# Kernel tuning notes

Hardware: AMD Instinct MI355X
Metric: run time of the kernel (lower is better)

The kernel has to match this reference:

```python
import jax, jax.numpy as jnp
import numpy as np

NEG_INF = -1e38

def wkv(w, u, k, v):
    """Numerically-stable RWKV-4 WKV recurrence.
    w, u: [C] (log-space decay / first-token bonus)
    k, v: [B, T, C]
    returns y: [B, T, C]
    """
    B, T, C = k.shape

    def step(carry, kv):
        p, q, o = carry          # numerator state, denominator state, running log-max; each [B, C]
        kt, vt = kv              # [B, C]
        # output at t (includes the u-boosted current token)
        no = jnp.maximum(o, u + kt)
        A = jnp.exp(o - no)
        Bt = jnp.exp(u + kt - no)
        y = (A * p + Bt * vt) / (A * q + Bt)
        # state update (decay by w, absorb current token)
        no2 = jnp.maximum(w + o, kt)
        A2 = jnp.exp(w + o - no2)
        B2 = jnp.exp(kt - no2)
        return (A2 * p + B2 * vt, A2 * q + B2, no2), y

    init = (jnp.zeros((B, C), k.dtype), jnp.zeros((B, C), k.dtype),
            jnp.full((B, C), NEG_INF, k.dtype))
    kT = jnp.swapaxes(k, 0, 1)   # [T, B, C]
    vT = jnp.swapaxes(v, 0, 1)
    _, ys = jax.lax.scan(step, init, (kT, vT))
    return jnp.swapaxes(ys, 0, 1)


def setup_inputs() -> dict:
    key = jax.random.key(0)
    ks = jax.random.split(key, 10)
    B, T, C = 8, 4096, 512
    scale = 1.0 / np.sqrt(C)
    return {
        "x": jax.random.normal(ks[0], (B, T, C), jnp.float32),
        "spatial_decay": jax.random.normal(ks[1], (C,), jnp.float32),
        "spatial_first": jax.random.normal(ks[2], (C,), jnp.float32),
        "mix_k": jax.random.uniform(ks[3], (1, 1, C), jnp.float32),
        "mix_v": jax.random.uniform(ks[4], (1, 1, C), jnp.float32),
        "mix_r": jax.random.uniform(ks[5], (1, 1, C), jnp.float32),
        "wk": jax.random.normal(ks[6], (C, C), jnp.float32) * scale,
        "wv": jax.random.normal(ks[7], (C, C), jnp.float32) * scale,
        "wr": jax.random.normal(ks[8], (C, C), jnp.float32) * scale,
        "wo": jax.random.normal(ks[9], (C, C), jnp.float32) * scale,
    }


def reference(x, spatial_decay, spatial_first, mix_k, mix_v, mix_r, wk, wv, wr, wo):
    B, T, C = x.shape
    # time_shift: xx[t] = x[t-1], xx[0] = 0  (ZeroPad2d((0,0,1,-1)))
    xx = jnp.pad(x, ((0, 0), (1, 0), (0, 0)))[:, :-1]
    xk = x * mix_k + xx * (1.0 - mix_k)
    xv = x * mix_v + xx * (1.0 - mix_v)
    xr = x * mix_r + xx * (1.0 - mix_r)
    k = jnp.einsum('btc,cd->btd', xk, wk)
    v = jnp.einsum('btc,cd->btd', xv, wv)
    r = jnp.einsum('btc,cd->btd', xr, wr)
    sr = jax.nn.sigmoid(r)
    y = wkv(spatial_decay / T, spatial_first / T, k, v)
    return jnp.einsum('btc,cd->btd', sr * y, wo)
```

## Files before the change

kernel.cpp:

```cpp
#include <hip/hip_runtime.h>

#define BB 8
#define TT 4096
#define CC 512
#define MM (BB * TT)
#define SS 128
#define LL 32

typedef short short8 __attribute__((ext_vector_type(8)));
typedef unsigned short ushort8 __attribute__((ext_vector_type(8)));
typedef float f32x4 __attribute__((ext_vector_type(4)));

__device__ __forceinline__ unsigned short f2bf(float f) {
    unsigned int u = __float_as_uint(f);
    u += 0x7FFFu + ((u >> 16) & 1u);
    return (unsigned short)(u >> 16);
}
__device__ __forceinline__ float bf2f(unsigned short h) {
    return __uint_as_float(((unsigned int)h) << 16);
}

__device__ __forceinline__ void gl_lds16(const void* g, void* l) {
    __builtin_amdgcn_global_load_lds(
        (__attribute__((address_space(1))) void*)(unsigned long long)g,
        (__attribute__((address_space(3))) void*)(unsigned int)(unsigned long long)l,
        16, 0, 0);
}

__device__ __forceinline__ ushort8 pack8(f32x4 a, f32x4 b) {
    ushort8 r;
    r[0] = f2bf(a.x); r[1] = f2bf(a.y); r[2] = f2bf(a.z); r[3] = f2bf(a.w);
    r[4] = f2bf(b.x); r[5] = f2bf(b.y); r[6] = f2bf(b.z); r[7] = f2bf(b.w);
    return r;
}

__global__ __launch_bounds__(256) void transpose_w(
    const float* __restrict__ wk, const float* __restrict__ wv,
    const float* __restrict__ wr, const float* __restrict__ wo,
    unsigned short* __restrict__ wT) {
    __shared__ float t[64][65];
    const int which = blockIdx.z;
    const float* src = (which == 0) ? wk : (which == 1) ? wv : (which == 2) ? wr : wo;
    const int k0 = blockIdx.y * 64;
    const int n0 = blockIdx.x * 64;
    const int r = threadIdx.x >> 6;
    const int c = threadIdx.x & 63;
#pragma unroll
    for (int p = 0; p < 16; ++p)
        t[p * 4 + r][c] = src[(size_t)(k0 + p * 4 + r) * CC + n0 + c];
    __syncthreads();
    unsigned short* dst = wT + (size_t)which * (CC * CC);
#pragma unroll
    for (int p = 0; p < 16; ++p)
        dst[(size_t)(n0 + p * 4 + r) * CC + k0 + c] = f2bf(t[c][p * 4 + r]);
}

__global__ __launch_bounds__(256) void mix_kvr(
    const float* __restrict__ x,
    const float* __restrict__ mixk, const float* __restrict__ mixv,
    const float* __restrict__ mixr,
    unsigned short* __restrict__ kx, unsigned short* __restrict__ vx,
    unsigned short* __restrict__ rx) {
    const int idx = blockIdx.x * 256 + threadIdx.x;
    const int row = idx >> 6;
    const int ch  = (idx & 63) * 8;
    const int t   = row & (TT - 1);
    const size_t off = (size_t)row * CC + ch;
    const float* xr = x + off;

    const f32x4 zero4 = {0.f, 0.f, 0.f, 0.f};
    const f32x4 one4  = {1.f, 1.f, 1.f, 1.f};

    f32x4 xc0 = ((const f32x4*)xr)[0];
    f32x4 xc1 = ((const f32x4*)xr)[1];
    f32x4 xp0 = zero4, xp1 = zero4;
    if (t != 0) {
        xp0 = ((const f32x4*)(xr - CC))[0];
        xp1 = ((const f32x4*)(xr - CC))[1];
    }

    f32x4 m0, m1;
    m0 = ((const f32x4*)(mixk + ch))[0];
    m1 = ((const f32x4*)(mixk + ch))[1];
    *(ushort8*)(kx + off) = pack8(xc0 * m0 + xp0 * (one4 - m0),
                                  xc1 * m1 + xp1 * (one4 - m1));
    m0 = ((const f32x4*)(mixv + ch))[0];
    m1 = ((const f32x4*)(mixv + ch))[1];
    *(ushort8*)(vx + off) = pack8(xc0 * m0 + xp0 * (one4 - m0),
                                  xc1 * m1 + xp1 * (one4 - m1));
    m0 = ((const f32x4*)(mixr + ch))[0];
    m1 = ((const f32x4*)(mixr + ch))[1];
    *(ushort8*)(rx + off) = pack8(xc0 * m0 + xp0 * (one4 - m0),
                                  xc1 * m1 + xp1 * (one4 - m1));
}

template <bool F32OUT>
__device__ __forceinline__ void gemm_body(
    const unsigned short* __restrict__ A,
    const unsigned short* __restrict__ Bw,
    void* __restrict__ OutP, const int sig,
    const int pm, const int pn) {
    __shared__ unsigned short As[3][128 * 32];
    __shared__ unsigned short Bs[3][256 * 32];

    const int tid = threadIdx.x;
    const int ar = tid >> 2;
    const int cg = (tid & 3) ^ ((tid >> 3) & 3);
    const unsigned short* agA = A  + (size_t)(pm * 128 + ar) * CC + cg * 8;
    const unsigned short* agB = Bw + (size_t)(pn * 256 + ar) * CC + cg * 8;

    const int w = tid >> 6, lane = tid & 63;
    const int wr = w >> 1, wc = w & 1;
    const int q = lane >> 4, l16 = lane & 15;
    const int sw = (q ^ ((l16 >> 1) & 3)) * 8;

    f32x4 acc[4][8];
#pragma unroll
    for (int i = 0; i < 4; i++)
#pragma unroll
        for (int j = 0; j < 8; j++) acc[i][j] = (f32x4){0.f, 0.f, 0.f, 0.f};

#define STG(bi, k0) do {                                                        \
    gl_lds16(agA + (k0), &As[bi][tid * 8]);                                     \
    gl_lds16(agA + (size_t)64 * CC + (k0), &As[bi][(256 + tid) * 8]);           \
    gl_lds16(agB + (k0),                    &Bs[bi][(0 * 256 + tid) * 8]);      \
    gl_lds16(agB + (size_t)64  * CC + (k0), &Bs[bi][(1 * 256 + tid) * 8]);      \
    gl_lds16(agB + (size_t)128 * CC + (k0), &Bs[bi][(2 * 256 + tid) * 8]);      \
    gl_lds16(agB + (size_t)192 * CC + (k0), &Bs[bi][(3 * 256 + tid) * 8]);      \
} while (0)

    STG(0, 0);
    STG(1, 32);

#pragma unroll
    for (int kt = 0; kt < 16; ++kt) {
        const int bi = kt % 3;
        if (kt + 2 < 16) STG((kt + 2) % 3, (kt + 2) * 32);

        if (kt < 14)       asm volatile("s_waitcnt vmcnt(12)" ::: "memory");
        else if (kt == 14) asm volatile("s_waitcnt vmcnt(6)" ::: "memory");
        else               asm volatile("s_waitcnt vmcnt(0)" ::: "memory");
        __builtin_amdgcn_s_barrier();

        short8 a[4], b[8];
#pragma unroll
        for (int i = 0; i < 4; i++)
            a[i] = *(const short8*)&As[bi][(wr * 64 + i * 16 + l16) * 32 + sw];
#pragma unroll
        for (int j = 0; j < 8; j++)
            b[j] = *(const short8*)&Bs[bi][(wc * 128 + j * 16 + l16) * 32 + sw];
        asm volatile("s_waitcnt lgkmcnt(0)" ::: "memory");
        __builtin_amdgcn_s_barrier();

        __builtin_amdgcn_s_setprio(1);
#pragma unroll
        for (int i = 0; i < 4; i++)
#pragma unroll
            for (int j = 0; j < 8; j++)
                acc[i][j] = __builtin_amdgcn_mfma_f32_16x16x32_bf16(a[i], b[j], acc[i][j], 0, 0, 0);
        __builtin_amdgcn_s_setprio(0);
    }
#undef STG

    const size_t rb = (size_t)pm * 128 + wr * 64;
    const int nb = pn * 256 + wc * 128;
    if constexpr (F32OUT) {
        float* Out = (float*)OutP;
#pragma unroll
        for (int i = 0; i < 4; i++)
#pragma unroll
            for (int j = 0; j < 8; j++)
#pragma unroll
                for (int ii = 0; ii < 4; ii++) {
                    const int m = i * 16 + q * 4 + ii;
                    const int n = nb + j * 16 + l16;
                    Out[(rb + m) * CC + n] = acc[i][j][ii];
                }
    } else {
        unsigned short* Out = (unsigned short*)OutP;
#pragma unroll
        for (int i = 0; i < 4; i++)
#pragma unroll
            for (int j = 0; j < 8; j++)
#pragma unroll
                for (int ii = 0; ii < 4; ii++) {
                    const int m = i * 16 + q * 4 + ii;
                    const int n = nb + j * 16 + l16;
                    float val = acc[i][j][ii];
                    if (sig) val = 1.0f / (1.0f + __expf(-val));
                    Out[(rb + m) * CC + n] = f2bf(val);
                }
    }
}

__global__ __launch_bounds__(256, 2) void gemm_kvr3(
    const unsigned short* __restrict__ wT,
    const unsigned short* __restrict__ A0, const unsigned short* __restrict__ A1,
    const unsigned short* __restrict__ A2,
    unsigned short* __restrict__ O0, unsigned short* __restrict__ O1,
    unsigned short* __restrict__ O2) {
    const int z = blockIdx.y;
    const int lin = blockIdx.x;
    const int wg = (lin & 7) * 64 + (lin >> 3);
    const int pm = wg >> 1, pn = wg & 1;
    const unsigned short* A = (z == 0) ? A0 : (z == 1) ? A1 : A2;
    unsigned short* O = (z == 0) ? O0 : (z == 1) ? O1 : O2;
    gemm_body<false>(A, wT + (size_t)z * (CC * CC), O, z == 2, pm, pn);
}

__global__ __launch_bounds__(256, 2) void gemm_out(
    const unsigned short* __restrict__ zb, const unsigned short* __restrict__ woT,
    float* __restrict__ out) {
    const int lin = blockIdx.x;
    const int wg = (lin & 7) * 64 + (lin >> 3);
    gemm_body<true>(zb, woT, out, 0, wg >> 1, wg & 1);
}

__global__ __launch_bounds__(256) void wkv_part1(
    const unsigned short* __restrict__ kb, const unsigned short* __restrict__ vb,
    const float* __restrict__ sd,
    float* __restrict__ sp_, float* __restrict__ sq_, float* __restrict__ so_) {
    const int idx = blockIdx.x * 256 + threadIdx.x;
    const int c = idx & (CC - 1);
    const int b = (idx >> 9) & (BB - 1);
    const int s = idx >> 12;
    const float w = sd[c] * (1.0f / (float)TT);
    const size_t base = ((size_t)b * TT + (size_t)s * LL) * CC + c;
    const unsigned short* kp = kb + base;
    const unsigned short* vp = vb + base;

    float p = 0.f, q = 0.f, o = -1e38f;
#pragma unroll 8
    for (int i = 0; i < LL; ++i) {
        const float kt = bf2f(kp[(size_t)i * CC]);
        const float vt = bf2f(vp[(size_t)i * CC]);
        const float no2 = fmaxf(w + o, kt);
        const float A2  = __expf(w + o - no2);
        const float B2  = __expf(kt - no2);
        p = A2 * p + B2 * vt;
        q = A2 * q + B2;
        o = no2;
    }
    sp_[idx] = p; sq_[idx] = q; so_[idx] = o;
}

__global__ __launch_bounds__(256) void wkv_part2(
    const float* __restrict__ sd,
    float* __restrict__ sp_, float* __restrict__ sq_, float* __restrict__ so_) {
    const int idx = blockIdx.x * 256 + threadIdx.x;
    const int c = idx & (CC - 1);
    const float wL = sd[c] * ((float)LL / (float)TT);

    float p = 0.f, q = 0.f, o = -1e38f;
    float lp = sp_[idx], lq = sq_[idx], lo = so_[idx];
    for (int s = 0; s < SS; ++s) {
        const int off = s * (BB * CC) + idx;
        float nlp = 0.f, nlq = 0.f, nlo = 0.f;
        if (s + 1 < SS) {
            nlp = sp_[off + BB * CC];
            nlq = sq_[off + BB * CC];
            nlo = so_[off + BB * CC];
        }
        sp_[off] = p; sq_[off] = q; so_[off] = o;
        const float no = fmaxf(o + wL, lo);
        const float A  = __expf(o + wL - no);
        const float Bc = __expf(lo - no);
        p = A * p + Bc * lp;
        q = A * q + Bc * lq;
        o = no;
        lp = nlp; lq = nlq; lo = nlo;
    }
}

__global__ __launch_bounds__(256) void wkv_part3(
    const unsigned short* __restrict__ kb, const unsigned short* __restrict__ vb,
    const unsigned short* __restrict__ srb,
    const float* __restrict__ sd, const float* __restrict__ sf,
    const float* __restrict__ sp_, const float* __restrict__ sq_,
    const float* __restrict__ so_,
    unsigned short* __restrict__ zb) {
    const int idx = blockIdx.x * 256 + threadIdx.x;
    const int c = idx & (CC - 1);
    const int b = (idx >> 9) & (BB - 1);
    const int s = idx >> 12;
    const float w = sd[c] * (1.0f / (float)TT);
    const float u = sf[c] * (1.0f / (float)TT);
    const size_t base = ((size_t)b * TT + (size_t)s * LL) * CC + c;
    const unsigned short* kp = kb + base;
    const unsigned short* vp = vb + base;
    const unsigned short* sp = srb + base;
    unsigned short* zp = zb + base;

    float p = sp_[idx], q = sq_[idx], o = so_[idx];
#pragma unroll 4
    for (int i = 0; i < LL; ++i) {
        const float kt = bf2f(kp[(size_t)i * CC]);
        const float vt = bf2f(vp[(size_t)i * CC]);
        const float sr = bf2f(sp[(size_t)i * CC]);

        const float no = fmaxf(o, u + kt);
        const float A  = __expf(o - no);
        const float Bt = __expf(u + kt - no);
        const float y  = (A * p + Bt * vt) / (A * q + Bt);
        zp[(size_t)i * CC] = f2bf(sr * y);

        const float no2 = fmaxf(w + o, kt);
        const float A2  = __expf(w + o - no2);
        const float B2  = __expf(kt - no2);
        p = A2 * p + B2 * vt;
        q = A2 * q + B2;
        o = no2;
    }
}

extern "C" void kernel_launch(void* const* d_in, const int* in_sizes, int n_in,
                              void* d_out, int out_size, void* d_ws, size_t ws_size,
                              hipStream_t stream) {
    const float* x  = (const float*)d_in[0];
    const float* sd = (const float*)d_in[1];
    const float* sf = (const float*)d_in[2];
    const float* mk = (const float*)d_in[3];
    const float* mv = (const float*)d_in[4];
    const float* mr = (const float*)d_in[5];
    const float* wk = (const float*)d_in[6];
    const float* wv = (const float*)d_in[7];
    const float* wr = (const float*)d_in[8];
    const float* wo = (const float*)d_in[9];
    float* out = (float*)d_out;

    char* ws = (char*)d_ws;
    unsigned short* wT = (unsigned short*)ws;
    unsigned short* b1 = wT + (size_t)4 * CC * CC;
    unsigned short* b2 = b1 + (size_t)MM * CC;
    unsigned short* b3 = b2 + (size_t)MM * CC;
    unsigned short* b4 = b3 + (size_t)MM * CC;
    unsigned short* b5 = b4 + (size_t)MM * CC;
    float* sp_ = (float*)(b5 + (size_t)MM * CC);
    float* sq_ = sp_ + (size_t)SS * BB * CC;
    float* so_ = sq_ + (size_t)SS * BB * CC;
    unsigned short* woT = wT + (size_t)3 * CC * CC;
    unsigned short* srS = (unsigned short*)d_out;

    transpose_w<<<dim3(8, 8, 4), 256, 0, stream>>>(wk, wv, wr, wo, wT);

    mix_kvr<<<dim3((MM * CC / 8) / 256), 256, 0, stream>>>(
        x, mk, mv, mr, b1, b2, b3);

    gemm_kvr3<<<dim3(512, 3), 256, 0, stream>>>(wT, b1, b2, b3, b4, b5, srS);

    wkv_part1<<<dim3((SS * BB * CC) / 256), 256, 0, stream>>>(b4, b5, sd, sp_, sq_, so_);
    wkv_part2<<<dim3((BB * CC) / 256), 256, 0, stream>>>(sd, sp_, sq_, so_);
    wkv_part3<<<dim3((SS * BB * CC) / 256), 256, 0, stream>>>(
        b4, b5, srS, sd, sf, sp_, sq_, so_, b1);

    gemm_out<<<dim3(512), 256, 0, stream>>>(b1, woT, out);
}
```

Before: 295.6 us.

## Enlarge GEMM tiles to 256x256 with 8 waves and interleaved LDS staging

Reworks the shared bf16 GEMM body from a 128x256 tile on 4 waves to a 256x256 tile on 8 waves, each wave owning a 128x64 subtile. Global-to-LDS staging of A and B is split and interleaved between two MFMA half-phases. Only one barrier per k-step remains, and the k loop is no longer unrolled. The three kvr GEMMs are flattened into one 1D grid with a new block-swizzle, and the output GEMM uses half as many blocks. This aims for more operand reuse per LDS byte and better overlap of loads with MFMA, at the cost of larger LDS use (about 96 KB per block, likely one block per CU) and fewer blocks to balance the load.

New measurement: 313.6 us. 6.1% more time.

```diff
diff --git a/kernel.cpp b/kernel.cpp
--- a/kernel.cpp
+++ b/kernel.cpp
@@ -100,76 +100,101 @@
     const unsigned short* __restrict__ Bw,
     void* __restrict__ OutP, const int sig,
     const int pm, const int pn) {
-    __shared__ unsigned short As[3][128 * 32];
+    __shared__ unsigned short As[3][256 * 32];
     __shared__ unsigned short Bs[3][256 * 32];
 
     const int tid = threadIdx.x;
-    const int ar = tid >> 2;
     const int cg = (tid & 3) ^ ((tid >> 3) & 3);
-    const unsigned short* agA = A  + (size_t)(pm * 128 + ar) * CC + cg * 8;
-    const unsigned short* agB = Bw + (size_t)(pn * 256 + ar) * CC + cg * 8;
-
-    const int w = tid >> 6, lane = tid & 63;
-    const int wr = w >> 1, wc = w & 1;
+    const unsigned short* agA = A  + (size_t)(pm * 256 + (tid >> 2)) * CC + cg * 8;
+    const unsigned short* agB = Bw + (size_t)(pn * 256 + (tid >> 2)) * CC + cg * 8;
+
+    const int wid = tid >> 6;
+    const int wr = wid >> 2, wc = wid & 3;
+    const int lane = tid & 63;
     const int q = lane >> 4, l16 = lane & 15;
     const int sw = (q ^ ((l16 >> 1) & 3)) * 8;
 
-    f32x4 acc[4][8];
-#pragma unroll
-    for (int i = 0; i < 4; i++)
-#pragma unroll
-        for (int j = 0; j < 8; j++) acc[i][j] = (f32x4){0.f, 0.f, 0.f, 0.f};
-
-#define STG(bi, k0) do {                                                        \
-    gl_lds16(agA + (k0), &As[bi][tid * 8]);                                     \
-    gl_lds16(agA + (size_t)64 * CC + (k0), &As[bi][(256 + tid) * 8]);           \
-    gl_lds16(agB + (k0),                    &Bs[bi][(0 * 256 + tid) * 8]);      \
-    gl_lds16(agB + (size_t)64  * CC + (k0), &Bs[bi][(1 * 256 + tid) * 8]);      \
-    gl_lds16(agB + (size_t)128 * CC + (k0), &Bs[bi][(2 * 256 + tid) * 8]);      \
-    gl_lds16(agB + (size_t)192 * CC + (k0), &Bs[bi][(3 * 256 + tid) * 8]);      \
+    const int aro = (wr * 128 + l16) * 32 + sw;
+    const int bro = (wc * 64 + l16) * 32 + sw;
+
+    f32x4 acc[8][4];
+#pragma unroll
+    for (int i = 0; i < 8; i++)
+#pragma unroll
+        for (int j = 0; j < 4; j++) acc[i][j] = (f32x4){0.f, 0.f, 0.f, 0.f};
+
+#define STG_A(bi_, ke) do {                                                   \
+    gl_lds16(agA + (ke), &As[bi_][tid * 8]);                                  \
+    gl_lds16(agA + (size_t)128 * CC + (ke), &As[bi_][4096 + tid * 8]);        \
 } while (0)
-
-    STG(0, 0);
-    STG(1, 32);
-
-#pragma unroll
-    for (int kt = 0; kt < 16; ++kt) {
-        const int bi = kt % 3;
-        if (kt + 2 < 16) STG((kt + 2) % 3, (kt + 2) * 32);
-
-        if (kt < 14)       asm volatile("s_waitcnt vmcnt(12)" ::: "memory");
-        else if (kt == 14) asm volatile("s_waitcnt vmcnt(6)" ::: "memory");
-        else               asm volatile("s_waitcnt vmcnt(0)" ::: "memory");
+#define STG_B(bi_, ke) do {                                                   \
+    gl_lds16(agB + (ke), &Bs[bi_][tid * 8]);                                  \
+    gl_lds16(agB + (size_t)128 * CC + (ke), &Bs[bi_][4096 + tid * 8]);        \
+} while (0)
+
+    STG_A(0, 0);  STG_B(0, 0);
+    STG_A(1, 32); STG_B(1, 32);
+
+    short8 bfr[4], af[4];
+
+#define KT_PHASES(bi_, DO_STAGE, ke) do {                                     \
+    const int bi2_ = (bi_) + 2 >= 3 ? (bi_) - 1 : (bi_) + 2;                  \
+    if (DO_STAGE) STG_A(bi2_, ke);                                            \
+    _Pragma("unroll")                                                         \
+    for (int j = 0; j < 4; ++j)                                               \
+        bfr[j] = *(const short8*)&Bs[bi_][bro + j * 512];                     \
+    _Pragma("unroll")                                                         \
+    for (int i = 0; i < 4; ++i)                                               \
+        af[i] = *(const short8*)&As[bi_][aro + i * 512];                      \
+    asm volatile("s_waitcnt lgkmcnt(0)" ::: "memory");                        \
+    __builtin_amdgcn_s_setprio(1);                                            \
+    _Pragma("unroll")                                                         \
+    for (int i = 0; i < 4; ++i)                                               \
+        _Pragma("unroll")                                                     \
+        for (int j = 0; j < 4; ++j)                                           \
+            acc[i][j] = __builtin_amdgcn_mfma_f32_16x16x32_bf16(              \
+                af[i], bfr[j], acc[i][j], 0, 0, 0);                           \
+    __builtin_amdgcn_s_setprio(0);                                            \
+    if (DO_STAGE) STG_B(bi2_, ke);                                            \
+    _Pragma("unroll")                                                         \
+    for (int i = 0; i < 4; ++i)                                               \
+        af[i] = *(const short8*)&As[bi_][aro + 2048 + i * 512];               \
+    asm volatile("s_waitcnt lgkmcnt(0)" ::: "memory");                        \
+    __builtin_amdgcn_s_setprio(1);                                            \
+    _Pragma("unroll")                                                         \
+    for (int i = 0; i < 4; ++i)                                               \
+        _Pragma("unroll")                                                     \
+        for (int j = 0; j < 4; ++j)                                           \
+            acc[4 + i][j] = __builtin_amdgcn_mfma_f32_16x16x32_bf16(          \
+                af[i], bfr[j], acc[4 + i][j], 0, 0, 0);                       \
+    __builtin_amdgcn_s_setprio(0);                                            \
+} while (0)
+
+    int bi = 0, ks = 64;
+#pragma unroll 1
+    for (int t = 0; t < 15; ++t) {
+        asm volatile("s_waitcnt vmcnt(4)" ::: "memory");
         __builtin_amdgcn_s_barrier();
-
-        short8 a[4], b[8];
-#pragma unroll
-        for (int i = 0; i < 4; i++)
-            a[i] = *(const short8*)&As[bi][(wr * 64 + i * 16 + l16) * 32 + sw];
-#pragma unroll
-        for (int j = 0; j < 8; j++)
-            b[j] = *(const short8*)&Bs[bi][(wc * 128 + j * 16 + l16) * 32 + sw];
-        asm volatile("s_waitcnt lgkmcnt(0)" ::: "memory");
-        __builtin_amdgcn_s_barrier();
-
-        __builtin_amdgcn_s_setprio(1);
-#pragma unroll
-        for (int i = 0; i < 4; i++)
-#pragma unroll
-            for (int j = 0; j < 8; j++)
-                acc[i][j] = __builtin_amdgcn_mfma_f32_16x16x32_bf16(a[i], b[j], acc[i][j], 0, 0, 0);
-        __builtin_amdgcn_s_setprio(0);
-    }
-#undef STG
-
-    const size_t rb = (size_t)pm * 128 + wr * 64;
-    const int nb = pn * 256 + wc * 128;
+        KT_PHASES(bi, (t < 14), ks);
+        ks += 32;
+        bi = (bi + 1 == 3) ? 0 : bi + 1;
+    }
+    asm volatile("s_waitcnt vmcnt(0)" ::: "memory");
+    __builtin_amdgcn_s_barrier();
+    KT_PHASES(bi, false, 0);
+
+#undef KT_PHASES
+#undef STG_A
+#undef STG_B
+
+    const size_t rb = (size_t)pm * 256 + wr * 128;
+    const int nb = pn * 256 + wc * 64;
     if constexpr (F32OUT) {
         float* Out = (float*)OutP;
 #pragma unroll
-        for (int i = 0; i < 4; i++)
-#pragma unroll
-            for (int j = 0; j < 8; j++)
+        for (int i = 0; i < 8; i++)
+#pragma unroll
+            for (int j = 0; j < 4; j++)
 #pragma unroll
                 for (int ii = 0; ii < 4; ii++) {
                     const int m = i * 16 + q * 4 + ii;
@@ -179,9 +204,9 @@
     } else {
         unsigned short* Out = (unsigned short*)OutP;
 #pragma unroll
-        for (int i = 0; i < 4; i++)
-#pragma unroll
-            for (int j = 0; j < 8; j++)
+        for (int i = 0; i < 8; i++)
+#pragma unroll
+            for (int j = 0; j < 4; j++)
 #pragma unroll
                 for (int ii = 0; ii < 4; ii++) {
                     const int m = i * 16 + q * 4 + ii;
@@ -193,26 +218,27 @@
     }
 }
 
-__global__ __launch_bounds__(256, 2) void gemm_kvr3(
+__global__ __launch_bounds__(512, 2) void gemm_kvr3(
     const unsigned short* __restrict__ wT,
     const unsigned short* __restrict__ A0, const unsigned short* __restrict__ A1,
     const unsigned short* __restrict__ A2,
     unsigned short* __restrict__ O0, unsigned short* __restrict__ O1,
     unsigned short* __restrict__ O2) {
-    const int z = blockIdx.y;
     const int lin = blockIdx.x;
-    const int wg = (lin & 7) * 64 + (lin >> 3);
-    const int pm = wg >> 1, pn = wg & 1;
+    const int wg = (lin & 7) * 96 + (lin >> 3);
+    const int z = wg >> 8;
+    const int r = wg & 255;
+    const int pm = r >> 1, pn = r & 1;
     const unsigned short* A = (z == 0) ? A0 : (z == 1) ? A1 : A2;
     unsigned short* O = (z == 0) ? O0 : (z == 1) ? O1 : O2;
     gemm_body<false>(A, wT + (size_t)z * (CC * CC), O, z == 2, pm, pn);
 }
 
-__global__ __launch_bounds__(256, 2) void gemm_out(
+__global__ __launch_bounds__(512, 2) void gemm_out(
     const unsigned short* __restrict__ zb, const unsigned short* __restrict__ woT,
     float* __restrict__ out) {
     const int lin = blockIdx.x;
-    const int wg = (lin & 7) * 64 + (lin >> 3);
+    const int wg = (lin & 7) * 32 + (lin >> 3);
     gemm_body<true>(zb, woT, out, 0, wg >> 1, wg & 1);
 }
 
@@ -346,12 +372,12 @@
     mix_kvr<<<dim3((MM * CC / 8) / 256), 256, 0, stream>>>(
         x, mk, mv, mr, b1, b2, b3);
 
-    gemm_kvr3<<<dim3(512, 3), 256, 0, stream>>>(wT, b1, b2, b3, b4, b5, srS);
+    gemm_kvr3<<<dim3(768), 512, 0, stream>>>(wT, b1, b2, b3, b4, b5, srS);
 
     wkv_part1<<<dim3((SS * BB * CC) / 256), 256, 0, stream>>>(b4, b5, sd, sp_, sq_, so_);
     wkv_part2<<<dim3((BB * CC) / 256), 256, 0, stream>>>(sd, sp_, sq_, so_);
     wkv_part3<<<dim3((SS * BB * CC) / 256), 256, 0, stream>>>(
         b4, b5, srS, sd, sf, sp_, sq_, so_, b1);
 
-    gemm_out<<<dim3(512), 256, 0, stream>>>(b1, woT, out);
-}
+    gemm_out<<<dim3(256), 512, 0, stream>>>(b1, woT, out);
+}
```

## Parallelize chunk-state scan with Hillis-Steele in LDS; merge weight transpose into mix

Applied to the files above, without the earlier changes.

The serial 128-step cross-chunk state scan, which ran on only 4096 threads, becomes a parallel log-depth inclusive scan in shared memory. Each (batch, channel) pair gets 128 threads, one per chunk, and the associative combine uses doubling decay factors. Separately, the weight transpose and token-mix kernels are merged into one launch to save a kernel launch and let the two overlap. The scan does more total work and adds barriers, and the combine order differs slightly, which may change float rounding.

Result: no change. 299.8 us (+1.4%).

```diff
diff --git a/kernel.cpp b/kernel.cpp
--- a/kernel.cpp
+++ b/kernel.cpp
@@ -34,37 +34,40 @@
     return r;
 }
 
-__global__ __launch_bounds__(256) void transpose_w(
-    const float* __restrict__ wk, const float* __restrict__ wv,
-    const float* __restrict__ wr, const float* __restrict__ wo,
-    unsigned short* __restrict__ wT) {
-    __shared__ float t[64][65];
-    const int which = blockIdx.z;
-    const float* src = (which == 0) ? wk : (which == 1) ? wv : (which == 2) ? wr : wo;
-    const int k0 = blockIdx.y * 64;
-    const int n0 = blockIdx.x * 64;
-    const int r = threadIdx.x >> 6;
-    const int c = threadIdx.x & 63;
-#pragma unroll
-    for (int p = 0; p < 16; ++p)
-        t[p * 4 + r][c] = src[(size_t)(k0 + p * 4 + r) * CC + n0 + c];
-    __syncthreads();
-    unsigned short* dst = wT + (size_t)which * (CC * CC);
-#pragma unroll
-    for (int p = 0; p < 16; ++p)
-        dst[(size_t)(n0 + p * 4 + r) * CC + k0 + c] = f2bf(t[c][p * 4 + r]);
-}
-
-__global__ __launch_bounds__(256) void mix_kvr(
+__global__ __launch_bounds__(256) void prep(
     const float* __restrict__ x,
     const float* __restrict__ mixk, const float* __restrict__ mixv,
     const float* __restrict__ mixr,
+    const float* __restrict__ wk, const float* __restrict__ wv,
+    const float* __restrict__ wr, const float* __restrict__ wo,
+    unsigned short* __restrict__ wT,
     unsigned short* __restrict__ kx, unsigned short* __restrict__ vx,
     unsigned short* __restrict__ rx) {
-    const int idx = blockIdx.x * 256 + threadIdx.x;
+    __shared__ float t[64][65];
+    if (blockIdx.x < 256) {
+        const int bid = blockIdx.x;
+        const int which = bid >> 6;
+        const int rem = bid & 63;
+        const int k0 = (rem >> 3) * 64;
+        const int n0 = (rem & 7) * 64;
+        const float* src = (which == 0) ? wk : (which == 1) ? wv
+                         : (which == 2) ? wr : wo;
+        const int r = threadIdx.x >> 6;
+        const int c = threadIdx.x & 63;
+#pragma unroll
+        for (int p = 0; p < 16; ++p)
+            t[p * 4 + r][c] = src[(size_t)(k0 + p * 4 + r) * CC + n0 + c];
+        __syncthreads();
+        unsigned short* dst = wT + (size_t)which * (CC * CC);
+#pragma unroll
+        for (int p = 0; p < 16; ++p)
+            dst[(size_t)(n0 + p * 4 + r) * CC + k0 + c] = f2bf(t[c][p * 4 + r]);
+        return;
+    }
+    const int idx = (blockIdx.x - 256) * 256 + threadIdx.x;
     const int row = idx >> 6;
     const int ch  = (idx & 63) * 8;
-    const int t   = row & (TT - 1);
+    const int tt  = row & (TT - 1);
     const size_t off = (size_t)row * CC + ch;
     const float* xr = x + off;
 
@@ -74,7 +77,7 @@
     f32x4 xc0 = ((const f32x4*)xr)[0];
     f32x4 xc1 = ((const f32x4*)xr)[1];
     f32x4 xp0 = zero4, xp1 = zero4;
-    if (t != 0) {
+    if (tt != 0) {
         xp0 = ((const f32x4*)(xr - CC))[0];
         xp1 = ((const f32x4*)(xr - CC))[1];
     }
@@ -244,32 +247,49 @@
     sp_[idx] = p; sq_[idx] = q; so_[idx] = o;
 }
 
-__global__ __launch_bounds__(256) void wkv_part2(
+__global__ __launch_bounds__(256) void wkv_scan(
     const float* __restrict__ sd,
     float* __restrict__ sp_, float* __restrict__ sq_, float* __restrict__ so_) {
-    const int idx = blockIdx.x * 256 + threadIdx.x;
-    const int c = idx & (CC - 1);
+    __shared__ float P[2][128], Q[2][128], O[2][128];
+    const int gsub = threadIdx.x >> 7;
+    const int s    = threadIdx.x & 127;
+    const int g    = blockIdx.x * 2 + gsub;
+    const int c    = g & (CC - 1);
     const float wL = sd[c] * ((float)LL / (float)TT);
-
-    float p = 0.f, q = 0.f, o = -1e38f;
-    float lp = sp_[idx], lq = sq_[idx], lo = so_[idx];
-    for (int s = 0; s < SS; ++s) {
-        const int off = s * (BB * CC) + idx;
-        float nlp = 0.f, nlq = 0.f, nlo = 0.f;
-        if (s + 1 < SS) {
-            nlp = sp_[off + BB * CC];
-            nlq = sq_[off + BB * CC];
-            nlo = so_[off + BB * CC];
+    const int stride = BB * CC;
+
+    float p = sp_[s * stride + g];
+    float q = sq_[s * stride + g];
+    float o = so_[s * stride + g];
+    P[gsub][s] = p; Q[gsub][s] = q; O[gsub][s] = o;
+
+    float dec = wL;
+#pragma unroll
+    for (int d = 0; d < 7; ++d) {
+        const int off = 1 << d;
+        __syncthreads();
+        float pl = 0.f, ql = 0.f, ol = -1e38f;
+        if (s >= off) {
+            pl = P[gsub][s - off]; ql = Q[gsub][s - off]; ol = O[gsub][s - off];
         }
-        sp_[off] = p; sq_[off] = q; so_[off] = o;
-        const float no = fmaxf(o + wL, lo);
-        const float A  = __expf(o + wL - no);
-        const float Bc = __expf(lo - no);
-        p = A * p + Bc * lp;
-        q = A * q + Bc * lq;
-        o = no;
-        lp = nlp; lq = nlq; lo = nlo;
-    }
+        __syncthreads();
+        if (s >= off) {
+            const float no = fmaxf(ol + dec, o);
+            const float Al = __expf(ol + dec - no);
+            const float Bc = __expf(o - no);
+            p = Al * pl + Bc * p;
+            q = Al * ql + Bc * q;
+            o = no;
+            P[gsub][s] = p; Q[gsub][s] = q; O[gsub][s] = o;
+        }
+        dec += dec;
+    }
+    __syncthreads();
+    float ep = 0.f, eq = 0.f, eo = -1e38f;
+    if (s > 0) { ep = P[gsub][s - 1]; eq = Q[gsub][s - 1]; eo = O[gsub][s - 1]; }
+    sp_[s * stride + g] = ep;
+    sq_[s * stride + g] = eq;
+    so_[s * stride + g] = eo;
 }
 
 __global__ __launch_bounds__(256) void wkv_part3(
@@ -341,15 +361,13 @@
     unsigned short* woT = wT + (size_t)3 * CC * CC;
     unsigned short* srS = (unsigned short*)d_out;
 
-    transpose_w<<<dim3(8, 8, 4), 256, 0, stream>>>(wk, wv, wr, wo, wT);
-
-    mix_kvr<<<dim3((MM * CC / 8) / 256), 256, 0, stream>>>(
-        x, mk, mv, mr, b1, b2, b3);
+    prep<<<dim3(256 + (MM * CC / 8) / 256), 256, 0, stream>>>(
+        x, mk, mv, mr, wk, wv, wr, wo, wT, b1, b2, b3);
 
     gemm_kvr3<<<dim3(512, 3), 256, 0, stream>>>(wT, b1, b2, b3, b4, b5, srS);
 
     wkv_part1<<<dim3((SS * BB * CC) / 256), 256, 0, stream>>>(b4, b5, sd, sp_, sq_, so_);
-    wkv_part2<<<dim3((BB * CC) / 256), 256, 0, stream>>>(sd, sp_, sq_, so_);
+    wkv_scan<<<dim3((BB * CC) / 2), 256, 0, stream>>>(sd, sp_, sq_, so_);
     wkv_part3<<<dim3((SS * BB * CC) / 256), 256, 0, stream>>>(
         b4, b5, srS, sd, sf, sp_, sq_, so_, b1);
 
```
